# Kernel tuning notes

Measured on AMD Instinct MI355X. Metric: run time of the kernel, lower is better.

## Reference

```python
import jax, jax.numpy as jnp
from jax import lax
import numpy as np

# --- d12 group tables (dihedral group of order 12 acting on the hex grid) ---
# 7 hexagonal taps embedded in a 3x3 grid: center + 6-ring in cyclic (60 deg) order.
_HEX_POS = [(1, 1), (0, 0), (0, 1), (1, 2), (2, 2), (2, 1), (1, 0)]
_HEX_FLAT = np.array([y * 3 + x for (y, x) in _HEX_POS], dtype=np.int32)  # slots in flattened 3x3


def _compose(a, b):
    # group elements (f, r): i -> (-1)^f * i + r (mod 6). a o b.
    f1, r1 = a
    f2, r2 = b
    return (f1 ^ f2, (r1 + (r2 if f1 == 0 else -r2)) % 6)


def _inv(a):
    f, r = a
    return (0, (-r) % 6) if f == 0 else (1, r)


def _group_tables():
    # perm[g, h] = index of g^{-1} o h  (orientation-channel permutation per output orientation g)
    # tap_src[g, k] = source tap index for target tap k under g^{-1} (kernel rotation/reflection)
    perm = np.zeros((12, 12), dtype=np.int32)
    tap_src = np.zeros((12, 7), dtype=np.int32)
    for g in range(12):
        f, r = divmod(g, 6)
        gi = _inv((f, r))
        for h in range(12):
            fh, rh = divmod(h, 6)
            rf, rr = _compose(gi, (fh, rh))
            perm[g, h] = rf * 6 + rr
        tap_src[g, 0] = 0
        for i in range(6):
            src = (i - r) % 6 if f == 0 else (r - i) % 6
            tap_src[g, 1 + i] = 1 + src
    return perm, tap_src


def _padding_basis(Hp, Wp):
    # (T, I, J): per orientation slot t and padded position (y,x), the source
    # (orientation, row, col). Interior = identity; border pixels are gathered from
    # the opposite chart edge with the orientation's rotation part shifted (+/-1)
    # to stitch icosahedral face boundaries.
    T = np.zeros((12, Hp, Wp), dtype=np.int32)
    I = np.zeros((12, Hp, Wp), dtype=np.int32)
    J = np.zeros((12, Hp, Wp), dtype=np.int32)
    for t in range(12):
        f, r = divmod(t, 6)
        for y in range(Hp):
            for x in range(Wp):
                sy, sx, dt = y, x, 0
                if x == 0:
                    sx, dt = Wp - 2, 1
                elif x == Wp - 1:
                    sx, dt = 1, -1
                if y == 0:
                    sy = Hp - 2
                elif y == Hp - 1:
                    sy = 1
                T[t, y, x] = f * 6 + (r + dt) % 6
                I[t, y, x] = sy
                J[t, y, x] = sx
    return T, I, J


def setup_inputs() -> dict:
    key = jax.random.key(0)
    k1, k2, k3 = jax.random.split(key, 3)
    B, Cin, O, H = 8, 16, 16, 64
    x = jax.random.normal(k1, (B, Cin * 12, H + 2, 5 * H + 2), dtype=jnp.float32)
    weight = jax.random.normal(k2, (O, Cin, 12, 7), dtype=jnp.float32) * 0.05
    bias = jax.random.normal(k3, (O,), dtype=jnp.float32) * 0.05
    return {"x": x, "weight": weight, "bias": bias}


def reference(x, weight, bias):
    O, Cin = weight.shape[0], weight.shape[1]
    B = x.shape[0]
    perm, tap_src = _group_tables()

    # apply_weight_basis: gather-expand (O, Cin, 12, 7) -> (O*12, Cin*12, 3, 3)
    taps = weight[:, :, perm, :]  # (O, Cin, 12g, 12h, 7): orientation-channel permutation
    idx = jnp.broadcast_to(jnp.asarray(tap_src)[None, None, :, None, :], taps.shape[:-1] + (7,))
    taps = jnp.take_along_axis(taps, idx, axis=-1)  # rotated/reflected taps per g
    K9 = jnp.zeros((O, Cin, 12, 12, 9), dtype=weight.dtype)
    K9 = K9.at[..., jnp.asarray(_HEX_FLAT)].set(taps)  # scatter 7 taps into 3x3 (corners stay 0)
    K = K9.reshape(O, Cin, 12, 12, 3, 3).transpose(0, 2, 1, 3, 4, 5).reshape(O * 12, Cin * 12, 3, 3)

    bias_e = jnp.repeat(bias, 12)  # bias[bias_basis]

    out = lax.conv_general_dilated(x, K, (1, 1), "VALID",
                                   dimension_numbers=("NCHW", "OIHW", "NCHW"))
    out = out + bias_e[None, :, None, None]

    # F.pad(out, (1,1,1,1)) then d12.pad: boundary-stitch gather with orientation permutation
    z = jnp.pad(out, ((0, 0), (0, 0), (1, 1), (1, 1)))
    Hp, Wp = z.shape[2], z.shape[3]
    T, I, J = _padding_basis(Hp, Wp)
    zr = z.reshape(B, O, 12, Hp, Wp)
    res = zr[:, :, jnp.asarray(T), jnp.asarray(I), jnp.asarray(J)]  # (B, O, 12, Hp, Wp)
    return res.reshape(B, O * 12, Hp, Wp)
```

## Files before the change

kernel.cpp:

```cpp
#include <hip/hip_runtime.h>

#define NB   8
#define NIC  192
#define NOC  192
#define HP   66
#define WP   322
#define HPWP (HP * WP)

typedef _Float16 f16x8 __attribute__((ext_vector_type(8)));
typedef float    f32x4 __attribute__((ext_vector_type(4)));

__device__ __align__(16) _Float16 g_Ks[6 * 7 * 12 * 64 * 8];
__device__ __align__(16) _Float16 g_xt[NB * 6 * 66 * 4 * 322 * 8];

#define ICCH  (66 * 4 * 322 * 8)
#define SLABH (12 * 64 * 8)

__global__ void prep_kernel(const float* __restrict__ w) {
    int tid = blockIdx.x * 256 + threadIdx.x;
    if (tid >= 7 * NOC * NIC) return;
    int ic = tid % NIC;
    int rest = tid / NIC;
    int oc = rest % NOC;
    int t = rest / NOC;
    int o = oc / 12, g = oc % 12;
    int c = ic / 12, h = ic % 12;
    int f = g / 6, r = g % 6;
    int ri = (f == 0) ? (6 - r) % 6 : r;
    int fh = h / 6, rh = h % 6;
    int pf = f ^ fh;
    int pr = (f == 0) ? (ri + rh) % 6 : (ri - rh + 6) % 6;
    int pm = pf * 6 + pr;
    const float* wsrc = w + ((o * 16 + c) * 12 + pm) * 7;
    float v;
    if (t == 0) {
        v = wsrc[0];
    } else {
        int i = t - 1;
        int s = (f == 0) ? (i - r + 6) % 6 : (r - i + 6) % 6;
        v = wsrc[1 + s];
    }
    int icc = ic >> 5, kg = (ic >> 3) & 3, j = ic & 7;
    int wn2 = oc / 96, mi = (oc % 96) / 16, n15 = oc % 16;
    g_Ks[((((icc * 7) + t) * 12 + mi * 2 + wn2) * 64 + kg * 16 + n15) * 8 + j]
        = (_Float16)v;
}

__global__ __launch_bounds__(256) void transpose_kernel(const float* __restrict__ x) {
    int id  = blockIdx.x;
    int y   = id % 66;
    int icc = (id / 66) % 6;
    int b   = id / 396;
    int kg   = threadIdx.x >> 6;
    int lane = threadIdx.x & 63;
    const float* src0 = x + ((size_t)b * NIC + icc * 32 + kg * 8) * HPWP + (size_t)y * WP;
    _Float16* dst = g_xt + ((((size_t)(b * 6 + icc) * 66 + y) * 4 + kg) * 322) * 8;
#pragma unroll
    for (int p = 0; p < 3; p++) {
        int c2 = lane + p * 64;
        if (p < 2 || c2 < 161) {
            float2 v[8];
#pragma unroll
            for (int j = 0; j < 8; j++)
                v[j] = *(const float2*)(src0 + (size_t)j * HPWP + c2 * 2);
            union { f16x8 a; _Float16 h[8]; } u0, u1;
#pragma unroll
            for (int j = 0; j < 8; j++) {
                u0.h[j] = (_Float16)v[j].x;
                u1.h[j] = (_Float16)v[j].y;
            }
            *(f16x8*)&dst[(c2 * 2 + 0) * 8] = u0.a;
            *(f16x8*)&dst[(c2 * 2 + 1) * 8] = u1.a;
        }
    }
}

__device__ __forceinline__ void gload16(const _Float16* g, _Float16* l) {
    __builtin_amdgcn_global_load_lds(
        (const __attribute__((address_space(1))) void*)g,
        (__attribute__((address_space(3))) void*)l, 16, 0, 0);
}

__global__ __launch_bounds__(256, 2) void conv_kernel(
    const float* __restrict__ bias, float* __restrict__ out) {
    __shared__ __align__(16) _Float16 lB[2][8960];

    int id = blockIdx.x;
    id = (id & 7) * 160 + (id >> 3);
    int xt5 = id % 5;
    int yt = (id / 5) % 32;
    int b  = id / 160;
    int px0 = xt5 * 64, py0 = yt * 2;

    int tid = threadIdx.x;
    int wave = tid >> 6;
    int lane = tid & 63;
    int kg = lane >> 4, n15 = lane & 15;
    int wm = wave & 1;
    int wn = wave >> 1;

    const int HY[7] = {1, 0, 0, 1, 2, 2, 1};
    const int HX[7] = {1, 0, 1, 2, 2, 1, 0};

    const _Float16* xtb = g_xt + (size_t)b * (6 * ICCH);
    int awo = (wn * 64 + lane) * 8;

    int gbo[5], lso[5];
#pragma unroll
    for (int k = 0; k < 5; k++) {
        int slot = tid + k * 256;
        if (slot > 1055) slot = 1055;
        int row = slot / 264;
        int rem = slot % 264;
        int kg2 = rem / 66;
        int col = rem % 66;
        gbo[k] = (((py0 + row) * 4 + kg2) * 322 + px0 + col) * 8;
        lso[k] = slot * 8;
    }

    f32x4 acc[6][4] = {};
    f16x8 aC[6], aN[6];

    {
        const _Float16* bsrc = xtb;
        gload16(bsrc + gbo[0], &lB[0][lso[0]]);
        gload16(bsrc + gbo[1], &lB[0][lso[1]]);
        gload16(bsrc + gbo[2], &lB[0][lso[2]]);
        gload16(bsrc + gbo[3], &lB[0][lso[3]]);
        gload16(bsrc + gbo[4], &lB[0][lso[4]]);
#pragma unroll
        for (int mi = 0; mi < 6; mi++)
            aC[mi] = *(const f16x8*)(g_Ks + awo + mi * 1024);
    }

    int bi = 0;
    for (int icc = 0; icc < 6; icc++) {
        __syncthreads();
        if (icc < 5) {
            const _Float16* bsrc = xtb + (size_t)(icc + 1) * ICCH;
            gload16(bsrc + gbo[0], &lB[bi ^ 1][lso[0]]);
            gload16(bsrc + gbo[1], &lB[bi ^ 1][lso[1]]);
            gload16(bsrc + gbo[2], &lB[bi ^ 1][lso[2]]);
            gload16(bsrc + gbo[3], &lB[bi ^ 1][lso[3]]);
            gload16(bsrc + gbo[4], &lB[bi ^ 1][lso[4]]);
        }
        const _Float16* ka = g_Ks + icc * (7 * SLABH);
#pragma unroll
        for (int t = 0; t < 7; t++) {
            if (t < 6 || icc < 5) {
                const _Float16* ap = ka + (t + 1) * SLABH + awo;
#pragma unroll
                for (int mi = 0; mi < 6; mi++)
                    aN[mi] = *(const f16x8*)(ap + mi * 1024);
            }
            const _Float16* bb = &lB[bi][(((wm + HY[t]) * 4 + kg) * 66 +
                                          HX[t] + n15) * 8];
            f16x8 xf[4];
#pragma unroll
            for (int ni = 0; ni < 4; ni++)
                xf[ni] = *(const f16x8*)(bb + ni * (16 * 8));
            __builtin_amdgcn_s_setprio(1);
#pragma unroll
            for (int mi = 0; mi < 6; mi++) {
#pragma unroll
                for (int ni = 0; ni < 4; ni++)
                    acc[mi][ni] = __builtin_amdgcn_mfma_f32_16x16x32_f16(
                        aC[mi], xf[ni], acc[mi][ni], 0, 0, 0);
            }
            __builtin_amdgcn_s_setprio(0);
#pragma unroll
            for (int mi = 0; mi < 6; mi++) aC[mi] = aN[mi];
        }
        bi ^= 1;
    }

    int yo = py0 + 1 + wm;
#pragma unroll
    for (int mi = 0; mi < 6; mi++) {
#pragma unroll
        for (int reg = 0; reg < 4; reg++) {
            int oc = wn * 96 + mi * 16 + kg * 4 + reg;
            float bv = bias[oc / 12];
            size_t base = ((size_t)(b * NOC + oc) * HP + yo) * WP + 1 + px0 + n15;
#pragma unroll
            for (int ni = 0; ni < 4; ni++)
                out[base + ni * 16] = acc[mi][ni][reg] + bv;
        }
    }
}

__global__ void border_kernel(float* __restrict__ out) {
    int tid = blockIdx.x * 256 + threadIdx.x;
    int r  = tid % 772;
    int bc = tid / 772;
    int ch = bc % NOC;
    int b  = bc / NOC;
    int y, xx;
    if (r < 322)      { y = 0;  xx = r; }
    else if (r < 644) { y = 65; xx = r - 322; }
    else if (r < 708) { xx = 0;   y = r - 644 + 1; }
    else              { xx = 321; y = r - 708 + 1; }
    int t = ch % 12;
    int o12 = ch - t;
    int f = t / 6, rr = t % 6;
    int dt = (xx == 0) ? 1 : ((xx == 321) ? -1 : 0);
    int sx = (xx == 0) ? 320 : ((xx == 321) ? 1 : xx);
    int sy = (y == 0) ? 64 : ((y == 65) ? 1 : y);
    int tsrc = f * 6 + (rr + dt + 6) % 6;
    float v = out[((size_t)(b * NOC + o12 + tsrc) * HP + sy) * WP + sx];
    out[((size_t)(b * NOC + ch) * HP + y) * WP + xx] = v;
}

extern "C" void kernel_launch(void* const* d_in, const int* in_sizes, int n_in,
                              void* d_out, int out_size, void* d_ws, size_t ws_size,
                              hipStream_t stream) {
    const float* x    = (const float*)d_in[0];
    const float* w    = (const float*)d_in[1];
    const float* bias = (const float*)d_in[2];
    float* out = (float*)d_out;

    prep_kernel<<<(7 * NOC * NIC + 255) / 256, 256, 0, stream>>>(w);
    transpose_kernel<<<NB * 6 * 66, 256, 0, stream>>>(x);
    conv_kernel<<<1280, 256, 0, stream>>>(bias, out);
    border_kernel<<<(NB * NOC * 772) / 256, 256, 0, stream>>>(out);
}
```

Baseline: 323.2 us.

## Fuse fp32-to-fp16 input transpose into conv kernel staging

Removes the separate transpose kernel and its fp16 global intermediate buffer. The conv kernel now reads fp32 input directly, converts it to fp16 in registers and writes it into LDS in the channel-interleaved layout. The next chunk is staged mid-loop to overlap with the MFMAs. This saves one kernel launch and a full write and read of the transposed input. In exchange it adds scattered 2-byte LDS stores, more VGPRs for the offset arrays, and redundant halo reads of fp32 data across tiles.

```diff
diff --git a/kernel.cpp b/kernel.cpp
--- a/kernel.cpp
+++ b/kernel.cpp
@@ -11,9 +11,7 @@
 typedef float    f32x4 __attribute__((ext_vector_type(4)));
 
 __device__ __align__(16) _Float16 g_Ks[6 * 7 * 12 * 64 * 8];
-__device__ __align__(16) _Float16 g_xt[NB * 6 * 66 * 4 * 322 * 8];
 
-#define ICCH  (66 * 4 * 322 * 8)
 #define SLABH (12 * 64 * 8)
 
 __global__ void prep_kernel(const float* __restrict__ w) {
@@ -46,44 +44,10 @@
         = (_Float16)v;
 }
 
-__global__ __launch_bounds__(256) void transpose_kernel(const float* __restrict__ x) {
-    int id  = blockIdx.x;
-    int y   = id % 66;
-    int icc = (id / 66) % 6;
-    int b   = id / 396;
-    int kg   = threadIdx.x >> 6;
-    int lane = threadIdx.x & 63;
-    const float* src0 = x + ((size_t)b * NIC + icc * 32 + kg * 8) * HPWP + (size_t)y * WP;
-    _Float16* dst = g_xt + ((((size_t)(b * 6 + icc) * 66 + y) * 4 + kg) * 322) * 8;
-#pragma unroll
-    for (int p = 0; p < 3; p++) {
-        int c2 = lane + p * 64;
-        if (p < 2 || c2 < 161) {
-            float2 v[8];
-#pragma unroll
-            for (int j = 0; j < 8; j++)
-                v[j] = *(const float2*)(src0 + (size_t)j * HPWP + c2 * 2);
-            union { f16x8 a; _Float16 h[8]; } u0, u1;
-#pragma unroll
-            for (int j = 0; j < 8; j++) {
-                u0.h[j] = (_Float16)v[j].x;
-                u1.h[j] = (_Float16)v[j].y;
-            }
-            *(f16x8*)&dst[(c2 * 2 + 0) * 8] = u0.a;
-            *(f16x8*)&dst[(c2 * 2 + 1) * 8] = u1.a;
-        }
-    }
-}
-
-__device__ __forceinline__ void gload16(const _Float16* g, _Float16* l) {
-    __builtin_amdgcn_global_load_lds(
-        (const __attribute__((address_space(1))) void*)g,
-        (__attribute__((address_space(3))) void*)l, 16, 0, 0);
-}
-
 __global__ __launch_bounds__(256, 2) void conv_kernel(
-    const float* __restrict__ bias, float* __restrict__ out) {
-    __shared__ __align__(16) _Float16 lB[2][8960];
+    const float* __restrict__ x, const float* __restrict__ bias,
+    float* __restrict__ out) {
+    __shared__ __align__(16) _Float16 lB[2][8448];
 
     int id = blockIdx.x;
     id = (id & 7) * 160 + (id >> 3);
@@ -102,48 +66,46 @@
     const int HY[7] = {1, 0, 0, 1, 2, 2, 1};
     const int HX[7] = {1, 0, 1, 2, 2, 1, 0};
 
-    const _Float16* xtb = g_xt + (size_t)b * (6 * ICCH);
     int awo = (wn * 64 + lane) * 8;
 
-    int gbo[5], lso[5];
+    int goff[17];
+    int lo[17];
 #pragma unroll
-    for (int k = 0; k < 5; k++) {
-        int slot = tid + k * 256;
-        if (slot > 1055) slot = 1055;
-        int row = slot / 264;
-        int rem = slot % 264;
-        int kg2 = rem / 66;
-        int col = rem % 66;
-        gbo[k] = (((py0 + row) * 4 + kg2) * 322 + px0 + col) * 8;
-        lso[k] = slot * 8;
+    for (int k = 0; k < 17; k++) {
+        int s = tid + k * 256;
+        if (s > 4223) s = 4223;
+        int row = s / 1056;
+        int rem = s % 1056;
+        int ic  = rem / 33;
+        int c2  = rem % 33;
+        int kg2 = ic >> 3, j = ic & 7;
+        goff[k] = ic * HPWP + row * WP + 2 * c2;
+        lo[k]   = (((row * 4 + kg2) * 66) + 2 * c2) * 8 + j;
+    }
+    const float* xs = x + ((size_t)b * NIC) * HPWP + (size_t)py0 * WP + px0;
+
+#define STAGE(ICC, DST)                                                        \
+    {                                                                          \
+        const float* _sp = xs + (size_t)(ICC) * 32 * HPWP;                     \
+        _Pragma("unroll")                                                      \
+        for (int k = 0; k < 17; k++) {                                         \
+            float2 v = *(const float2*)(_sp + goff[k]);                        \
+            (DST)[lo[k]]     = (_Float16)v.x;                                  \
+            (DST)[lo[k] + 8] = (_Float16)v.y;                                  \
+        }                                                                      \
     }
 
     f32x4 acc[6][4] = {};
     f16x8 aC[6], aN[6];
 
-    {
-        const _Float16* bsrc = xtb;
-        gload16(bsrc + gbo[0], &lB[0][lso[0]]);
-        gload16(bsrc + gbo[1], &lB[0][lso[1]]);
-        gload16(bsrc + gbo[2], &lB[0][lso[2]]);
-        gload16(bsrc + gbo[3], &lB[0][lso[3]]);
-        gload16(bsrc + gbo[4], &lB[0][lso[4]]);
+    STAGE(0, lB[0]);
 #pragma unroll
-        for (int mi = 0; mi < 6; mi++)
-            aC[mi] = *(const f16x8*)(g_Ks + awo + mi * 1024);
-    }
+    for (int mi = 0; mi < 6; mi++)
+        aC[mi] = *(const f16x8*)(g_Ks + awo + mi * 1024);
+    __syncthreads();
 
     int bi = 0;
     for (int icc = 0; icc < 6; icc++) {
-        __syncthreads();
-        if (icc < 5) {
-            const _Float16* bsrc = xtb + (size_t)(icc + 1) * ICCH;
-            gload16(bsrc + gbo[0], &lB[bi ^ 1][lso[0]]);
-            gload16(bsrc + gbo[1], &lB[bi ^ 1][lso[1]]);
-            gload16(bsrc + gbo[2], &lB[bi ^ 1][lso[2]]);
-            gload16(bsrc + gbo[3], &lB[bi ^ 1][lso[3]]);
-            gload16(bsrc + gbo[4], &lB[bi ^ 1][lso[4]]);
-        }
         const _Float16* ka = g_Ks + icc * (7 * SLABH);
 #pragma unroll
         for (int t = 0; t < 7; t++) {
@@ -152,6 +114,9 @@
 #pragma unroll
                 for (int mi = 0; mi < 6; mi++)
                     aN[mi] = *(const f16x8*)(ap + mi * 1024);
+            }
+            if (t == 1 && icc < 5) {
+                STAGE(icc + 1, lB[bi ^ 1]);
             }
             const _Float16* bb = &lB[bi][(((wm + HY[t]) * 4 + kg) * 66 +
                                           HX[t] + n15) * 8];
@@ -171,6 +136,7 @@
 #pragma unroll
             for (int mi = 0; mi < 6; mi++) aC[mi] = aN[mi];
         }
+        __syncthreads();
         bi ^= 1;
     }
 
@@ -187,6 +153,7 @@
                 out[base + ni * 16] = acc[mi][ni][reg] + bv;
         }
     }
+#undef STAGE
 }
 
 __global__ void border_kernel(float* __restrict__ out) {
@@ -220,7 +187,6 @@
     float* out = (float*)d_out;
 
     prep_kernel<<<(7 * NOC * NIC + 255) / 256, 256, 0, stream>>>(w);
-    transpose_kernel<<<NB * 6 * 66, 256, 0, stream>>>(x);
-    conv_kernel<<<1280, 256, 0, stream>>>(bias, out);
+    conv_kernel<<<1280, 256, 0, stream>>>(x, bias, out);
     border_kernel<<<(NB * NOC * 772) / 256, 256, 0, stream>>>(out);
 }
```

After: 313.8 us. -2.9%, faster.
